# Performance work log

Hardware: AMD Instinct MI355X
Metric: run time of the kernel (lower is better)

Reference implementation:

```python
import jax, jax.numpy as jnp
import numpy as np

N_NODES = 100000
N_EDGES = 1600000
IN_DIM = 128
HID = 64
N_CLASSES = 40
NEG_SLOPE = 0.2


def setup_inputs() -> dict:
    key = jax.random.key(0)
    ks = jax.random.split(key, 12)
    s_in = 1.0 / np.sqrt(IN_DIM)
    s_h = 1.0 / np.sqrt(HID)
    return {
        "x": jax.random.normal(ks[0], (N_NODES, IN_DIM), dtype=jnp.float32),
        "edge_index": jax.random.randint(ks[1], (2, N_EDGES), 0, N_NODES, dtype=jnp.int64),
        "W0": jax.random.normal(ks[2], (IN_DIM, HID), dtype=jnp.float32) * s_in,
        "a_s0": jax.random.normal(ks[3], (HID,), dtype=jnp.float32) * s_h,
        "a_d0": jax.random.normal(ks[4], (HID,), dtype=jnp.float32) * s_h,
        "b0": jnp.zeros((HID,), dtype=jnp.float32),
        "W1": jax.random.normal(ks[5], (HID, HID), dtype=jnp.float32) * s_h,
        "a_s1": jax.random.normal(ks[6], (HID,), dtype=jnp.float32) * s_h,
        "a_d1": jax.random.normal(ks[7], (HID,), dtype=jnp.float32) * s_h,
        "b1": jnp.zeros((HID,), dtype=jnp.float32),
        "Wl": jax.random.normal(ks[8], (HID, N_CLASSES), dtype=jnp.float32) * s_h,
        "bl": jnp.zeros((N_CLASSES,), dtype=jnp.float32),
    }


def gat_conv(x, src, dst, W, a_s, a_d, b, n_nodes):
    # single-head GATConv (PyG default heads=1), self-loops already in src/dst
    h = x @ W                                  # [N, d]
    e = jax.nn.leaky_relu((h @ a_s)[src] + (h @ a_d)[dst], NEG_SLOPE)  # [E]
    # segment softmax over incoming edges of each dst node
    m = jax.ops.segment_max(e, dst, num_segments=n_nodes)
    p = jnp.exp(e - m[dst])
    denom = jax.ops.segment_sum(p, dst, num_segments=n_nodes)
    alpha = p / (denom[dst] + 1e-16)           # [E]
    out = jax.ops.segment_sum(alpha[:, None] * h[src], dst, num_segments=n_nodes)
    return out + b


def reference(x, edge_index, W0, a_s0, a_d0, b0, W1, a_s1, a_d1, b1, Wl, bl):
    n = x.shape[0]
    loop = jnp.arange(n, dtype=edge_index.dtype)
    src = jnp.concatenate([edge_index[0], loop])
    dst = jnp.concatenate([edge_index[1], loop])
    h = gat_conv(x, src, dst, W0, a_s0, a_d0, b0, n)
    h = jax.nn.elu(h)
    h = gat_conv(h, src, dst, W1, a_s1, a_d1, b1, n)
    h = jax.nn.elu(h)
    return h @ Wl + bl
```

## Files before the change

### kernel.cpp

```cpp
#include <hip/hip_runtime.h>
#include <math.h>

#define NEG_SLOPE 0.2f
#define CAP 256
#define BSH 9
#define BSZ 512
#define CHUNK 2048
#define PADS 16

typedef __attribute__((ext_vector_type(8))) short short8;
typedef __attribute__((ext_vector_type(4))) float f32x4;

__device__ __forceinline__ float hred_sum(float v) {
#pragma unroll
    for (int o = 16; o >= 1; o >>= 1) v += __shfl_xor(v, o, 64);
    return v;
}
__device__ __forceinline__ unsigned int f2bf(float f) {
    unsigned int u = __float_as_uint(f);
    return (u + 0x7fffu + ((u >> 16) & 1u)) >> 16;
}
__device__ __forceinline__ float bflo(unsigned int u) { return __uint_as_float(u << 16); }
__device__ __forceinline__ float bfhi(unsigned int u) { return __uint_as_float(u & 0xffff0000u); }


__global__ __launch_bounds__(256) void k_zero(int* p, int n) {
    int i = blockIdx.x * 256 + threadIdx.x;
    if (i < n) p[i] = 0;
}

__global__ __launch_bounds__(256) void k_hist(const int* __restrict__ dst, int* __restrict__ bcount, int E) {
    __shared__ int lh[256];
    lh[threadIdx.x] = 0;
    __syncthreads();
    int gid = blockIdx.x * 256 + threadIdx.x;
    int nth = gridDim.x * 256;
    int E4 = E >> 2;
    for (int i = gid; i < E4; i += nth) {
        int4 d = ((const int4*)dst)[i];
        atomicAdd(&lh[d.x >> BSH], 1);
        atomicAdd(&lh[d.y >> BSH], 1);
        atomicAdd(&lh[d.z >> BSH], 1);
        atomicAdd(&lh[d.w >> BSH], 1);
    }
    for (int i = (E4 << 2) + gid; i < E; i += nth)
        atomicAdd(&lh[dst[i] >> BSH], 1);
    __syncthreads();
    int c = lh[threadIdx.x];
    if (c) atomicAdd(&bcount[threadIdx.x * PADS], c);
}

__global__ __launch_bounds__(256) void k_bscan(const int* __restrict__ bcount,
                                               int* __restrict__ eoff, int* __restrict__ boff,
                                               int* __restrict__ bcursor, int* __restrict__ rowptr,
                                               int nbuck, int N, int E) {
    __shared__ int s1[256], s2[256];
    int t = threadIdx.x;
    int bc = (t < nbuck) ? bcount[t * PADS] : 0;
    int cn = 0;
    if (t < nbuck) { cn = N - (t << BSH); if (cn > BSZ) cn = BSZ; if (cn < 0) cn = 0; }
    int tot = bc + cn;
    s1[t] = bc; s2[t] = tot;
    __syncthreads();
#pragma unroll
    for (int off = 1; off < 256; off <<= 1) {
        int u1 = (t >= off) ? s1[t - off] : 0;
        int u2 = (t >= off) ? s2[t - off] : 0;
        __syncthreads();
        s1[t] += u1; s2[t] += u2;
        __syncthreads();
    }
    if (t < nbuck) {
        int e = s1[t] - bc, b = s2[t] - tot;
        eoff[t] = e; boff[t] = b; bcursor[t * PADS] = e;
    }
    if (t == 0) rowptr[N] = E + N;
}

__global__ __launch_bounds__(256) void k_scatter(const int* __restrict__ src, const int* __restrict__ dst,
                                                 int* __restrict__ bcursor, int* __restrict__ ebuf, int E) {
    __shared__ int lh[256], lb[256];
    const int tid = threadIdx.x;
    int base = blockIdx.x * CHUNK;
    int sv[8], dv[8];
    bool ok[8];
#pragma unroll
    for (int u = 0; u < 8; ++u) {
        int i = base + u * 256 + tid;
        ok[u] = i < E;
        int ii = ok[u] ? i : E - 1;
        dv[u] = dst[ii];
        sv[u] = src[ii];
    }
    lh[tid] = 0;
    __syncthreads();
#pragma unroll
    for (int u = 0; u < 8; ++u)
        if (ok[u]) atomicAdd(&lh[dv[u] >> BSH], 1);
    __syncthreads();
    int c = lh[tid];
    lb[tid] = c ? atomicAdd(&bcursor[tid * PADS], c) : 0;
    lh[tid] = 0;
    __syncthreads();
#pragma unroll
    for (int u = 0; u < 8; ++u) {
        if (ok[u]) {
            int d = dv[u], b = d >> BSH;
            int p = atomicAdd(&lh[b], 1);
            ebuf[lb[b] + p] = (sv[u] << BSH) | (d & (BSZ - 1));
        }
    }
}

__global__ __launch_bounds__(512) void k_build(const int* __restrict__ eoff, const int* __restrict__ boff,
                                               const int* __restrict__ bcount, const int* __restrict__ ebuf,
                                               int* __restrict__ rowptr, int* __restrict__ csr, int N) {
    __shared__ int sdeg[BSZ], sscan[BSZ];
    int b = blockIdx.x, t = threadIdx.x;
    int nlo = b << BSH;
    int cn = N - nlo; if (cn > BSZ) cn = BSZ;
    int e0 = eoff[b], ec = bcount[b * PADS], cb = boff[b];
    sdeg[t] = (t < cn) ? 1 : 0;
    __syncthreads();
    {
        int i = t;
        for (; i + 1536 < ec; i += 2048) {
            int r0 = ebuf[e0 + i], r1 = ebuf[e0 + i + 512];
            int r2 = ebuf[e0 + i + 1024], r3 = ebuf[e0 + i + 1536];
            atomicAdd(&sdeg[r0 & (BSZ - 1)], 1);
            atomicAdd(&sdeg[r1 & (BSZ - 1)], 1);
            atomicAdd(&sdeg[r2 & (BSZ - 1)], 1);
            atomicAdd(&sdeg[r3 & (BSZ - 1)], 1);
        }
        for (; i < ec; i += 512)
            atomicAdd(&sdeg[ebuf[e0 + i] & (BSZ - 1)], 1);
    }
    __syncthreads();
    int v = sdeg[t];
    sscan[t] = v;
    __syncthreads();
#pragma unroll
    for (int off = 1; off < BSZ; off <<= 1) {
        int u = (t >= off) ? sscan[t - off] : 0;
        __syncthreads();
        sscan[t] += u;
        __syncthreads();
    }
    int excl = sscan[t] - v;
    if (t < cn) {
        rowptr[nlo + t] = cb + excl;
        csr[cb + excl] = nlo + t;
        sdeg[t] = excl + 1;
    }
    __syncthreads();
    {
        int i = t;
        for (; i + 1536 < ec; i += 2048) {
            int r0 = ebuf[e0 + i], r1 = ebuf[e0 + i + 512];
            int r2 = ebuf[e0 + i + 1024], r3 = ebuf[e0 + i + 1536];
            int p0 = atomicAdd(&sdeg[r0 & (BSZ - 1)], 1);
            int p1 = atomicAdd(&sdeg[r1 & (BSZ - 1)], 1);
            int p2 = atomicAdd(&sdeg[r2 & (BSZ - 1)], 1);
            int p3 = atomicAdd(&sdeg[r3 & (BSZ - 1)], 1);
            csr[cb + p0] = r0 >> BSH;
            csr[cb + p1] = r1 >> BSH;
            csr[cb + p2] = r2 >> BSH;
            csr[cb + p3] = r3 >> BSH;
        }
        for (; i < ec; i += 512) {
            int rec = ebuf[e0 + i];
            int p = atomicAdd(&sdeg[rec & (BSZ - 1)], 1);
            csr[cb + p] = rec >> BSH;
        }
    }
}


template <int K, int OUTW, bool SS, bool HB>
__global__ __launch_bounds__(256) void k_gemm(const float* __restrict__ X,
                                              const float* __restrict__ W,
                                              const float* __restrict__ a_s,
                                              const float* __restrict__ a_d,
                                              const float* __restrict__ bias,
                                              void* __restrict__ Hout,
                                              float* __restrict__ ss,
                                              float* __restrict__ sd, int N) {
    constexpr int NKC = K / 32;
    constexpr int NC  = (OUTW + 15) / 16;
    __shared__ __align__(16) short wfrag[NKC * NC * 64 * 8];
    __shared__ __align__(16) unsigned int hs[HB ? 4 : 1][16 * 32];

    const int tid  = threadIdx.x;
    const int lane = tid & 63;
    const int w    = tid >> 6;
    const int m    = lane & 15;
    const int q8   = lane >> 4;
    const int rowbase = blockIdx.x * 64 + w * 16;

    for (int f = tid; f < NKC * NC * 64; f += 256) {
        int flane = f & 63;
        int fc    = (f >> 6) % NC;
        int fkc   = (f >> 6) / NC;
        int col   = fc * 16 + (flane & 15);
        int k0    = fkc * 32 + (flane >> 4) * 8;
        short8 b;
#pragma unroll
        for (int j = 0; j < 8; ++j) {
            float v = (col < OUTW) ? W[(k0 + j) * OUTW + col] : 0.f;
            b[j] = (short)f2bf(v);
        }
        *(short8*)&wfrag[f * 8] = b;
    }
    __syncthreads();

    int grow = rowbase + m; if (grow >= N) grow = N - 1;
    const float* xrow = X + (size_t)grow * K + q8 * 8;

    f32x4 acc[NC];
#pragma unroll
    for (int c = 0; c < NC; ++c) acc[c] = (f32x4)0.f;

#pragma unroll
    for (int kc = 0; kc < NKC; ++kc) {
        float4 v0 = *(const float4*)(xrow + kc * 32);
        float4 v1 = *(const float4*)(xrow + kc * 32 + 4);
        float vv[8] = {v0.x, v0.y, v0.z, v0.w, v1.x, v1.y, v1.z, v1.w};
        short8 ah, al;
#pragma unroll
        for (int j = 0; j < 8; ++j) {
            unsigned int hb16 = f2bf(vv[j]);
            ah[j] = (short)hb16;
            al[j] = (short)f2bf(vv[j] - __uint_as_float(hb16 << 16));
        }
#pragma unroll
        for (int c = 0; c < NC; ++c) {
            short8 b = *(short8*)&wfrag[((kc * NC + c) * 64 + lane) * 8];
            acc[c] = __builtin_amdgcn_mfma_f32_16x16x32_bf16(ah, b, acc[c], 0, 0, 0);
            acc[c] = __builtin_amdgcn_mfma_f32_16x16x32_bf16(al, b, acc[c], 0, 0, 0);
        }
    }

    if (SS) {
        float asv[NC], adv[NC];
#pragma unroll
        for (int c = 0; c < NC; ++c) { asv[c] = a_s[c * 16 + m]; adv[c] = a_d[c * 16 + m]; }
#pragma unroll
        for (int i = 0; i < 4; ++i) {
            float s = 0.f, d = 0.f;
#pragma unroll
            for (int c = 0; c < NC; ++c) {
                s = fmaf(acc[c][i], asv[c], s);
                d = fmaf(acc[c][i], adv[c], d);
            }
#pragma unroll
            for (int o = 1; o <= 8; o <<= 1) {
                s += __shfl_xor(s, o, 64);
                d += __shfl_xor(d, o, 64);
            }
            int r = rowbase + q8 * 4 + i;
            if (m == 0 && r < N) { ss[r] = s; sd[r] = d; }
        }
    }

    if (HB) {
        unsigned short* hsw = (unsigned short*)&hs[w][0];
#pragma unroll
        for (int c = 0; c < NC; ++c)
#pragma unroll
            for (int i = 0; i < 4; ++i)
                hsw[(q8 * 4 + i) * 64 + c * 16 + m] = (unsigned short)f2bf(acc[c][i]);
        unsigned int* hu = &hs[w][0];
        int row = lane >> 2, u0 = (lane & 3) * 8;
        uint4 va = *(uint4*)&hu[row * 32 + u0];
        uint4 vb = *(uint4*)&hu[row * 32 + u0 + 4];
        int r = rowbase + row;
        if (r < N) {
            unsigned int* hbp = (unsigned int*)Hout;
            *(uint4*)&hbp[(size_t)r * 32 + u0]     = va;
            *(uint4*)&hbp[(size_t)r * 32 + u0 + 4] = vb;
        }
    } else {
        float bv[NC];
#pragma unroll
        for (int c = 0; c < NC; ++c) {
            int col = c * 16 + m;
            bv[c] = (col < OUTW) ? bias[col] : 0.f;
        }
        float* O = (float*)Hout;
#pragma unroll
        for (int i = 0; i < 4; ++i) {
            int r = rowbase + q8 * 4 + i;
            if (r < N) {
#pragma unroll
                for (int c = 0; c < NC; ++c) {
                    int col = c * 16 + m;
                    if (col < OUTW) O[(size_t)r * OUTW + col] = acc[c][i] + bv[c];
                }
            }
        }
    }
}


__global__ __launch_bounds__(256) void k_agg(const int* __restrict__ rowptr, const int* __restrict__ csr,
                                             const float* __restrict__ ss, const float* __restrict__ sd,
                                             const unsigned int* __restrict__ hb, const float* __restrict__ bias,
                                             float* __restrict__ z, int N) {
    __shared__ float2 ps[8 * CAP];
    const int tid = threadIdx.x;
    const int hw  = tid >> 5;
    const int p   = tid & 31;
    const int n   = blockIdx.x * 8 + hw;
    const bool valid = n < N;
    float2* myps = ps + hw * CAP;
    const char* hbb = (const char*)hb;
    const int p4 = p * 4;

    int ro = 0, deg = 0;
    float sdn = 0.f;
    if (valid) {
        ro  = rowptr[n];
        deg = rowptr[n + 1] - ro;
        sdn = sd[n];
    }

    if (deg <= CAP) {
        float sum = 0.f;
        for (int j = p; j < deg; j += 32) {
            int s = csr[ro + j];
            float e = ss[s] + sdn;
            e = fmaxf(e, NEG_SLOPE * e);
            float pe = __expf(e);
            myps[j] = make_float2(pe, __int_as_float(s << 7));
            sum += pe;
        }
        sum = hred_sum(sum);
        float inv = 1.f / (sum + 1e-16f);

        float ax = 0.f, ay = 0.f, bx = 0.f, by = 0.f, cx = 0.f, cy = 0.f, dx = 0.f, dy = 0.f;
        int j = 0;
        for (; j + 7 < deg; j += 8) {
            float2 e0 = myps[j],     e1 = myps[j + 1], e2 = myps[j + 2], e3 = myps[j + 3];
            float2 e4 = myps[j + 4], e5 = myps[j + 5], e6 = myps[j + 6], e7 = myps[j + 7];
            unsigned int u0 = *(const unsigned int*)(hbb + (__float_as_int(e0.y) + p4));
            unsigned int u1 = *(const unsigned int*)(hbb + (__float_as_int(e1.y) + p4));
            unsigned int u2 = *(const unsigned int*)(hbb + (__float_as_int(e2.y) + p4));
            unsigned int u3 = *(const unsigned int*)(hbb + (__float_as_int(e3.y) + p4));
            unsigned int u4 = *(const unsigned int*)(hbb + (__float_as_int(e4.y) + p4));
            unsigned int u5 = *(const unsigned int*)(hbb + (__float_as_int(e5.y) + p4));
            unsigned int u6 = *(const unsigned int*)(hbb + (__float_as_int(e6.y) + p4));
            unsigned int u7 = *(const unsigned int*)(hbb + (__float_as_int(e7.y) + p4));
            ax = fmaf(bflo(u0), e0.x, ax); ay = fmaf(bfhi(u0), e0.x, ay);
            bx = fmaf(bflo(u1), e1.x, bx); by = fmaf(bfhi(u1), e1.x, by);
            cx = fmaf(bflo(u2), e2.x, cx); cy = fmaf(bfhi(u2), e2.x, cy);
            dx = fmaf(bflo(u3), e3.x, dx); dy = fmaf(bfhi(u3), e3.x, dy);
            ax = fmaf(bflo(u4), e4.x, ax); ay = fmaf(bfhi(u4), e4.x, ay);
            bx = fmaf(bflo(u5), e5.x, bx); by = fmaf(bfhi(u5), e5.x, by);
            cx = fmaf(bflo(u6), e6.x, cx); cy = fmaf(bfhi(u6), e6.x, cy);
            dx = fmaf(bflo(u7), e7.x, dx); dy = fmaf(bfhi(u7), e7.x, dy);
        }
        for (; j + 3 < deg; j += 4) {
            float2 e0 = myps[j], e1 = myps[j + 1], e2 = myps[j + 2], e3 = myps[j + 3];
            unsigned int u0 = *(const unsigned int*)(hbb + (__float_as_int(e0.y) + p4));
            unsigned int u1 = *(const unsigned int*)(hbb + (__float_as_int(e1.y) + p4));
            unsigned int u2 = *(const unsigned int*)(hbb + (__float_as_int(e2.y) + p4));
            unsigned int u3 = *(const unsigned int*)(hbb + (__float_as_int(e3.y) + p4));
            ax = fmaf(bflo(u0), e0.x, ax); ay = fmaf(bfhi(u0), e0.x, ay);
            bx = fmaf(bflo(u1), e1.x, bx); by = fmaf(bfhi(u1), e1.x, by);
            cx = fmaf(bflo(u2), e2.x, cx); cy = fmaf(bfhi(u2), e2.x, cy);
            dx = fmaf(bflo(u3), e3.x, dx); dy = fmaf(bfhi(u3), e3.x, dy);
        }
        for (; j < deg; ++j) {
            float2 e0 = myps[j];
            unsigned int u0 = *(const unsigned int*)(hbb + (__float_as_int(e0.y) + p4));
            ax = fmaf(bflo(u0), e0.x, ax); ay = fmaf(bfhi(u0), e0.x, ay);
        }
        float fx = (ax + bx) + (cx + dx);
        float fy = (ay + by) + (cy + dy);
        if (valid) {
            float2 ob = *(const float2*)&bias[p * 2];
            float ox = fmaf(fx, inv, ob.x);
            float oy = fmaf(fy, inv, ob.y);
            ox = (ox > 0.f) ? ox : __expf(ox) - 1.f;
            oy = (oy > 0.f) ? oy : __expf(oy) - 1.f;
            *(float2*)&z[(size_t)n * 64 + p * 2] = make_float2(ox, oy);
        }
    } else {
        float sum = 0.f;
        for (int j = p; j < deg; j += 32) {
            int s = csr[ro + j];
            float e = ss[s] + sdn;
            e = fmaxf(e, NEG_SLOPE * e);
            sum += __expf(e);
        }
        sum = hred_sum(sum);
        float inv = 1.f / (sum + 1e-16f);
        float fx = 0.f, fy = 0.f;
        for (int j = 0; j < deg; ++j) {
            int s = csr[ro + j];
            float e = ss[s] + sdn;
            e = fmaxf(e, NEG_SLOPE * e);
            float pe = __expf(e);
            unsigned int u = *(const unsigned int*)(hbb + ((s << 7) + p4));
            fx = fmaf(bflo(u), pe, fx); fy = fmaf(bfhi(u), pe, fy);
        }
        float2 ob = *(const float2*)&bias[p * 2];
        float ox = fmaf(fx, inv, ob.x);
        float oy = fmaf(fy, inv, ob.y);
        ox = (ox > 0.f) ? ox : __expf(ox) - 1.f;
        oy = (oy > 0.f) ? oy : __expf(oy) - 1.f;
        *(float2*)&z[(size_t)n * 64 + p * 2] = make_float2(ox, oy);
    }
}


extern "C" void kernel_launch(void* const* d_in, const int* in_sizes, int n_in,
                              void* d_out, int out_size, void* d_ws, size_t ws_size,
                              hipStream_t stream) {
    const float* x   = (const float*)d_in[0];
    const int*   ei  = (const int*)d_in[1];
    const float* W0  = (const float*)d_in[2];
    const float* as0 = (const float*)d_in[3];
    const float* ad0 = (const float*)d_in[4];
    const float* b0  = (const float*)d_in[5];
    const float* W1  = (const float*)d_in[6];
    const float* as1 = (const float*)d_in[7];
    const float* ad1 = (const float*)d_in[8];
    const float* b1  = (const float*)d_in[9];
    const float* Wl  = (const float*)d_in[10];
    const float* bl  = (const float*)d_in[11];
    float* out = (float*)d_out;

    int N = in_sizes[0] / 128;
    int E = in_sizes[1] / 2;
    const int* srcp = ei;
    const int* dstp = ei + E;
    int nbuck = (N + BSZ - 1) >> BSH;

    char* wp = (char*)d_ws;
    auto alloc = [&](size_t bytes) { void* p = (void*)wp; wp += (bytes + 255) & ~(size_t)255; return p; };
    unsigned int* hb = (unsigned int*)alloc((size_t)N * 32 * 4);
    float* z       = (float*)alloc((size_t)N * 64 * 4);
    float* ssb     = (float*)alloc((size_t)N * 4);
    float* sdb     = (float*)alloc((size_t)N * 4);
    int*   rowptr  = (int*)alloc((size_t)(N + 1) * 4);
    int*   csr     = (int*)alloc((size_t)(E + N) * 4);
    int*   ebuf    = (int*)alloc((size_t)E * 4);
    int*   bcount  = (int*)alloc(256 * PADS * 4);
    int*   eoff    = (int*)alloc(256 * 4);
    int*   boff    = (int*)alloc(256 * 4);
    int*   bcursor = (int*)alloc(256 * PADS * 4);

    k_zero<<<(256 * PADS + 255) / 256, 256, 0, stream>>>(bcount, 256 * PADS);
    k_hist<<<256, 256, 0, stream>>>(dstp, bcount, E);
    k_bscan<<<1, 256, 0, stream>>>(bcount, eoff, boff, bcursor, rowptr, nbuck, N, E);
    k_scatter<<<(E + CHUNK - 1) / CHUNK, 256, 0, stream>>>(srcp, dstp, bcursor, ebuf, E);
    k_build<<<nbuck, 512, 0, stream>>>(eoff, boff, bcount, ebuf, rowptr, csr, N);

    int gb = (N + 63) / 64;
    k_gemm<128, 64, true, true><<<gb, 256, 0, stream>>>(x, W0, as0, ad0, nullptr, hb, ssb, sdb, N);
    k_agg<<<(N + 7) / 8, 256, 0, stream>>>(rowptr, csr, ssb, sdb, hb, b0, z, N);
    k_gemm<64, 64, true, true><<<gb, 256, 0, stream>>>(z, W1, as1, ad1, nullptr, hb, ssb, sdb, N);
    k_agg<<<(N + 7) / 8, 256, 0, stream>>>(rowptr, csr, ssb, sdb, hb, b1, z, N);
    k_gemm<64, 40, false, false><<<gb, 256, 0, stream>>>(z, Wl, nullptr, nullptr, bl, out, nullptr, nullptr, N);
}
```

Before: 271.5 us.

## Store aggregation outputs as bf16 and drop atomic histogram reduction

The aggregation kernel now writes its ELU outputs as packed bf16 instead of fp32. The following GEMMs read that bf16 directly and issue one MFMA per tile instead of a hi/lo split pair. This halves intermediate traffic and MFMA work but lowers activation precision. The histogram now writes per-block partials that the scan kernel sums, removing the zero kernel and global atomics. The aggregation's shared-memory staging is split into separate weight and offset arrays so it can use vector loads.

```diff
diff --git a/kernel.cpp b/kernel.cpp
--- a/kernel.cpp
+++ b/kernel.cpp
@@ -7,6 +7,7 @@
 #define BSZ 512
 #define CHUNK 2048
 #define PADS 16
+#define HGRID 256
 
 typedef __attribute__((ext_vector_type(8))) short short8;
 typedef __attribute__((ext_vector_type(4))) float f32x4;
@@ -24,12 +25,7 @@
 __device__ __forceinline__ float bfhi(unsigned int u) { return __uint_as_float(u & 0xffff0000u); }
 
 
-__global__ __launch_bounds__(256) void k_zero(int* p, int n) {
-    int i = blockIdx.x * 256 + threadIdx.x;
-    if (i < n) p[i] = 0;
-}
-
-__global__ __launch_bounds__(256) void k_hist(const int* __restrict__ dst, int* __restrict__ bcount, int E) {
+__global__ __launch_bounds__(256) void k_hist(const int* __restrict__ dst, int* __restrict__ bpart, int E) {
     __shared__ int lh[256];
     lh[threadIdx.x] = 0;
     __syncthreads();
@@ -46,17 +42,24 @@
     for (int i = (E4 << 2) + gid; i < E; i += nth)
         atomicAdd(&lh[dst[i] >> BSH], 1);
     __syncthreads();
-    int c = lh[threadIdx.x];
-    if (c) atomicAdd(&bcount[threadIdx.x * PADS], c);
-}
-
-__global__ __launch_bounds__(256) void k_bscan(const int* __restrict__ bcount,
+    bpart[blockIdx.x * 256 + threadIdx.x] = lh[threadIdx.x];
+}
+
+__global__ __launch_bounds__(256) void k_bscan(const int* __restrict__ bpart,
                                                int* __restrict__ eoff, int* __restrict__ boff,
-                                               int* __restrict__ bcursor, int* __restrict__ rowptr,
+                                               int* __restrict__ bcursor, int* __restrict__ ecnt,
+                                               int* __restrict__ rowptr,
                                                int nbuck, int N, int E) {
     __shared__ int s1[256], s2[256];
     int t = threadIdx.x;
-    int bc = (t < nbuck) ? bcount[t * PADS] : 0;
+    int bc = 0;
+    for (int b = 0; b < HGRID; b += 4) {
+        bc += bpart[(b + 0) * 256 + t];
+        bc += bpart[(b + 1) * 256 + t];
+        bc += bpart[(b + 2) * 256 + t];
+        bc += bpart[(b + 3) * 256 + t];
+    }
+    if (t >= nbuck) bc = 0;
     int cn = 0;
     if (t < nbuck) { cn = N - (t << BSH); if (cn > BSZ) cn = BSZ; if (cn < 0) cn = 0; }
     int tot = bc + cn;
@@ -72,7 +75,7 @@
     }
     if (t < nbuck) {
         int e = s1[t] - bc, b = s2[t] - tot;
-        eoff[t] = e; boff[t] = b; bcursor[t * PADS] = e;
+        eoff[t] = e; boff[t] = b; ecnt[t] = bc; bcursor[t * PADS] = e;
     }
     if (t == 0) rowptr[N] = E + N;
 }
@@ -113,13 +116,13 @@
 }
 
 __global__ __launch_bounds__(512) void k_build(const int* __restrict__ eoff, const int* __restrict__ boff,
-                                               const int* __restrict__ bcount, const int* __restrict__ ebuf,
+                                               const int* __restrict__ ecnt, const int* __restrict__ ebuf,
                                                int* __restrict__ rowptr, int* __restrict__ csr, int N) {
     __shared__ int sdeg[BSZ], sscan[BSZ];
     int b = blockIdx.x, t = threadIdx.x;
     int nlo = b << BSH;
     int cn = N - nlo; if (cn > BSZ) cn = BSZ;
-    int e0 = eoff[b], ec = bcount[b * PADS], cb = boff[b];
+    int e0 = eoff[b], ec = ecnt[b], cb = boff[b];
     sdeg[t] = (t < cn) ? 1 : 0;
     __syncthreads();
     {
@@ -176,8 +179,8 @@
 }
 
 
-template <int K, int OUTW, bool SS, bool HB>
-__global__ __launch_bounds__(256) void k_gemm(const float* __restrict__ X,
+template <int K, int OUTW, bool SS, bool HB, bool XB>
+__global__ __launch_bounds__(256) void k_gemm(const void* __restrict__ X,
                                               const float* __restrict__ W,
                                               const float* __restrict__ a_s,
                                               const float* __restrict__ a_d,
@@ -214,29 +217,42 @@
     __syncthreads();
 
     int grow = rowbase + m; if (grow >= N) grow = N - 1;
-    const float* xrow = X + (size_t)grow * K + q8 * 8;
 
     f32x4 acc[NC];
 #pragma unroll
     for (int c = 0; c < NC; ++c) acc[c] = (f32x4)0.f;
 
-#pragma unroll
-    for (int kc = 0; kc < NKC; ++kc) {
-        float4 v0 = *(const float4*)(xrow + kc * 32);
-        float4 v1 = *(const float4*)(xrow + kc * 32 + 4);
-        float vv[8] = {v0.x, v0.y, v0.z, v0.w, v1.x, v1.y, v1.z, v1.w};
-        short8 ah, al;
-#pragma unroll
-        for (int j = 0; j < 8; ++j) {
-            unsigned int hb16 = f2bf(vv[j]);
-            ah[j] = (short)hb16;
-            al[j] = (short)f2bf(vv[j] - __uint_as_float(hb16 << 16));
-        }
-#pragma unroll
-        for (int c = 0; c < NC; ++c) {
-            short8 b = *(short8*)&wfrag[((kc * NC + c) * 64 + lane) * 8];
-            acc[c] = __builtin_amdgcn_mfma_f32_16x16x32_bf16(ah, b, acc[c], 0, 0, 0);
-            acc[c] = __builtin_amdgcn_mfma_f32_16x16x32_bf16(al, b, acc[c], 0, 0, 0);
+    if (XB) {
+        const unsigned short* xrow = (const unsigned short*)X + (size_t)grow * 64 + q8 * 8;
+#pragma unroll
+        for (int kc = 0; kc < NKC; ++kc) {
+            short8 ah = *(const short8*)(xrow + kc * 32);
+#pragma unroll
+            for (int c = 0; c < NC; ++c) {
+                short8 b = *(short8*)&wfrag[((kc * NC + c) * 64 + lane) * 8];
+                acc[c] = __builtin_amdgcn_mfma_f32_16x16x32_bf16(ah, b, acc[c], 0, 0, 0);
+            }
+        }
+    } else {
+        const float* xrow = (const float*)X + (size_t)grow * K + q8 * 8;
+#pragma unroll
+        for (int kc = 0; kc < NKC; ++kc) {
+            float4 v0 = *(const float4*)(xrow + kc * 32);
+            float4 v1 = *(const float4*)(xrow + kc * 32 + 4);
+            float vv[8] = {v0.x, v0.y, v0.z, v0.w, v1.x, v1.y, v1.z, v1.w};
+            short8 ah, al;
+#pragma unroll
+            for (int j = 0; j < 8; ++j) {
+                unsigned int hb16 = f2bf(vv[j]);
+                ah[j] = (short)hb16;
+                al[j] = (short)f2bf(vv[j] - __uint_as_float(hb16 << 16));
+            }
+#pragma unroll
+            for (int c = 0; c < NC; ++c) {
+                short8 b = *(short8*)&wfrag[((kc * NC + c) * 64 + lane) * 8];
+                acc[c] = __builtin_amdgcn_mfma_f32_16x16x32_bf16(ah, b, acc[c], 0, 0, 0);
+                acc[c] = __builtin_amdgcn_mfma_f32_16x16x32_bf16(al, b, acc[c], 0, 0, 0);
+            }
         }
     }
 
@@ -305,14 +321,14 @@
 __global__ __launch_bounds__(256) void k_agg(const int* __restrict__ rowptr, const int* __restrict__ csr,
                                              const float* __restrict__ ss, const float* __restrict__ sd,
                                              const unsigned int* __restrict__ hb, const float* __restrict__ bias,
-                                             float* __restrict__ z, int N) {
-    __shared__ float2 ps[8 * CAP];
+                                             unsigned int* __restrict__ z, int N) {
+    __shared__ __align__(16) float sal[8][CAP];
+    __shared__ __align__(16) int   sof[8][CAP];
     const int tid = threadIdx.x;
     const int hw  = tid >> 5;
     const int p   = tid & 31;
     const int n   = blockIdx.x * 8 + hw;
     const bool valid = n < N;
-    float2* myps = ps + hw * CAP;
     const char* hbb = (const char*)hb;
     const int p4 = p * 4;
 
@@ -331,7 +347,8 @@
             float e = ss[s] + sdn;
             e = fmaxf(e, NEG_SLOPE * e);
             float pe = __expf(e);
-            myps[j] = make_float2(pe, __int_as_float(s << 7));
+            sal[hw][j] = pe;
+            sof[hw][j] = s << 7;
             sum += pe;
         }
         sum = hred_sum(sum);
@@ -340,40 +357,43 @@
         float ax = 0.f, ay = 0.f, bx = 0.f, by = 0.f, cx = 0.f, cy = 0.f, dx = 0.f, dy = 0.f;
         int j = 0;
         for (; j + 7 < deg; j += 8) {
-            float2 e0 = myps[j],     e1 = myps[j + 1], e2 = myps[j + 2], e3 = myps[j + 3];
-            float2 e4 = myps[j + 4], e5 = myps[j + 5], e6 = myps[j + 6], e7 = myps[j + 7];
-            unsigned int u0 = *(const unsigned int*)(hbb + (__float_as_int(e0.y) + p4));
-            unsigned int u1 = *(const unsigned int*)(hbb + (__float_as_int(e1.y) + p4));
-            unsigned int u2 = *(const unsigned int*)(hbb + (__float_as_int(e2.y) + p4));
-            unsigned int u3 = *(const unsigned int*)(hbb + (__float_as_int(e3.y) + p4));
-            unsigned int u4 = *(const unsigned int*)(hbb + (__float_as_int(e4.y) + p4));
-            unsigned int u5 = *(const unsigned int*)(hbb + (__float_as_int(e5.y) + p4));
-            unsigned int u6 = *(const unsigned int*)(hbb + (__float_as_int(e6.y) + p4));
-            unsigned int u7 = *(const unsigned int*)(hbb + (__float_as_int(e7.y) + p4));
-            ax = fmaf(bflo(u0), e0.x, ax); ay = fmaf(bfhi(u0), e0.x, ay);
-            bx = fmaf(bflo(u1), e1.x, bx); by = fmaf(bfhi(u1), e1.x, by);
-            cx = fmaf(bflo(u2), e2.x, cx); cy = fmaf(bfhi(u2), e2.x, cy);
-            dx = fmaf(bflo(u3), e3.x, dx); dy = fmaf(bfhi(u3), e3.x, dy);
-            ax = fmaf(bflo(u4), e4.x, ax); ay = fmaf(bfhi(u4), e4.x, ay);
-            bx = fmaf(bflo(u5), e5.x, bx); by = fmaf(bfhi(u5), e5.x, by);
-            cx = fmaf(bflo(u6), e6.x, cx); cy = fmaf(bfhi(u6), e6.x, cy);
-            dx = fmaf(bflo(u7), e7.x, dx); dy = fmaf(bfhi(u7), e7.x, dy);
+            float4 al0 = *(const float4*)&sal[hw][j];
+            float4 al1 = *(const float4*)&sal[hw][j + 4];
+            int4   of0 = *(const int4*)&sof[hw][j];
+            int4   of1 = *(const int4*)&sof[hw][j + 4];
+            unsigned int u0 = *(const unsigned int*)(hbb + (of0.x + p4));
+            unsigned int u1 = *(const unsigned int*)(hbb + (of0.y + p4));
+            unsigned int u2 = *(const unsigned int*)(hbb + (of0.z + p4));
+            unsigned int u3 = *(const unsigned int*)(hbb + (of0.w + p4));
+            unsigned int u4 = *(const unsigned int*)(hbb + (of1.x + p4));
+            unsigned int u5 = *(const unsigned int*)(hbb + (of1.y + p4));
+            unsigned int u6 = *(const unsigned int*)(hbb + (of1.z + p4));
+            unsigned int u7 = *(const unsigned int*)(hbb + (of1.w + p4));
+            ax = fmaf(bflo(u0), al0.x, ax); ay = fmaf(bfhi(u0), al0.x, ay);
+            bx = fmaf(bflo(u1), al0.y, bx); by = fmaf(bfhi(u1), al0.y, by);
+            cx = fmaf(bflo(u2), al0.z, cx); cy = fmaf(bfhi(u2), al0.z, cy);
+            dx = fmaf(bflo(u3), al0.w, dx); dy = fmaf(bfhi(u3), al0.w, dy);
+            ax = fmaf(bflo(u4), al1.x, ax); ay = fmaf(bfhi(u4), al1.x, ay);
+            bx = fmaf(bflo(u5), al1.y, bx); by = fmaf(bfhi(u5), al1.y, by);
+            cx = fmaf(bflo(u6), al1.z, cx); cy = fmaf(bfhi(u6), al1.z, cy);
+            dx = fmaf(bflo(u7), al1.w, dx); dy = fmaf(bfhi(u7), al1.w, dy);
         }
         for (; j + 3 < deg; j += 4) {
-            float2 e0 = myps[j], e1 = myps[j + 1], e2 = myps[j + 2], e3 = myps[j + 3];
-            unsigned int u0 = *(const unsigned int*)(hbb + (__float_as_int(e0.y) + p4));
-            unsigned int u1 = *(const unsigned int*)(hbb + (__float_as_int(e1.y) + p4));
-            unsigned int u2 = *(const unsigned int*)(hbb + (__float_as_int(e2.y) + p4));
-            unsigned int u3 = *(const unsigned int*)(hbb + (__float_as_int(e3.y) + p4));
-            ax = fmaf(bflo(u0), e0.x, ax); ay = fmaf(bfhi(u0), e0.x, ay);
-            bx = fmaf(bflo(u1), e1.x, bx); by = fmaf(bfhi(u1), e1.x, by);
-            cx = fmaf(bflo(u2), e2.x, cx); cy = fmaf(bfhi(u2), e2.x, cy);
-            dx = fmaf(bflo(u3), e3.x, dx); dy = fmaf(bfhi(u3), e3.x, dy);
+            float4 al0 = *(const float4*)&sal[hw][j];
+            int4   of0 = *(const int4*)&sof[hw][j];
+            unsigned int u0 = *(const unsigned int*)(hbb + (of0.x + p4));
+            unsigned int u1 = *(const unsigned int*)(hbb + (of0.y + p4));
+            unsigned int u2 = *(const unsigned int*)(hbb + (of0.z + p4));
+            unsigned int u3 = *(const unsigned int*)(hbb + (of0.w + p4));
+            ax = fmaf(bflo(u0), al0.x, ax); ay = fmaf(bfhi(u0), al0.x, ay);
+            bx = fmaf(bflo(u1), al0.y, bx); by = fmaf(bfhi(u1), al0.y, by);
+            cx = fmaf(bflo(u2), al0.z, cx); cy = fmaf(bfhi(u2), al0.z, cy);
+            dx = fmaf(bflo(u3), al0.w, dx); dy = fmaf(bfhi(u3), al0.w, dy);
         }
         for (; j < deg; ++j) {
-            float2 e0 = myps[j];
-            unsigned int u0 = *(const unsigned int*)(hbb + (__float_as_int(e0.y) + p4));
-            ax = fmaf(bflo(u0), e0.x, ax); ay = fmaf(bfhi(u0), e0.x, ay);
+            float a = sal[hw][j];
+            unsigned int u0 = *(const unsigned int*)(hbb + (sof[hw][j] + p4));
+            ax = fmaf(bflo(u0), a, ax); ay = fmaf(bfhi(u0), a, ay);
         }
         float fx = (ax + bx) + (cx + dx);
         float fy = (ay + by) + (cy + dy);
@@ -383,7 +403,7 @@
             float oy = fmaf(fy, inv, ob.y);
             ox = (ox > 0.f) ? ox : __expf(ox) - 1.f;
             oy = (oy > 0.f) ? oy : __expf(oy) - 1.f;
-            *(float2*)&z[(size_t)n * 64 + p * 2] = make_float2(ox, oy);
+            z[(size_t)n * 32 + p] = (f2bf(oy) << 16) | f2bf(ox);
         }
     } else {
         float sum = 0.f;
@@ -409,7 +429,7 @@
         float oy = fmaf(fy, inv, ob.y);
         ox = (ox > 0.f) ? ox : __expf(ox) - 1.f;
         oy = (oy > 0.f) ? oy : __expf(oy) - 1.f;
-        *(float2*)&z[(size_t)n * 64 + p * 2] = make_float2(ox, oy);
+        z[(size_t)n * 32 + p] = (f2bf(oy) << 16) | f2bf(ox);
     }
 }
 
@@ -440,27 +460,27 @@
     char* wp = (char*)d_ws;
     auto alloc = [&](size_t bytes) { void* p = (void*)wp; wp += (bytes + 255) & ~(size_t)255; return p; };
     unsigned int* hb = (unsigned int*)alloc((size_t)N * 32 * 4);
-    float* z       = (float*)alloc((size_t)N * 64 * 4);
+    unsigned int* z  = (unsigned int*)alloc((size_t)N * 32 * 4);
     float* ssb     = (float*)alloc((size_t)N * 4);
     float* sdb     = (float*)alloc((size_t)N * 4);
     int*   rowptr  = (int*)alloc((size_t)(N + 1) * 4);
     int*   csr     = (int*)alloc((size_t)(E + N) * 4);
     int*   ebuf    = (int*)alloc((size_t)E * 4);
-    int*   bcount  = (int*)alloc(256 * PADS * 4);
+    int*   bpart   = (int*)alloc((size_t)HGRID * 256 * 4);
     int*   eoff    = (int*)alloc(256 * 4);
     int*   boff    = (int*)alloc(256 * 4);
+    int*   ecnt    = (int*)alloc(256 * 4);
     int*   bcursor = (int*)alloc(256 * PADS * 4);
 
-    k_zero<<<(256 * PADS + 255) / 256, 256, 0, stream>>>(bcount, 256 * PADS);
-    k_hist<<<256, 256, 0, stream>>>(dstp, bcount, E);
-    k_bscan<<<1, 256, 0, stream>>>(bcount, eoff, boff, bcursor, rowptr, nbuck, N, E);
+    k_hist<<<HGRID, 256, 0, stream>>>(dstp, bpart, E);
+    k_bscan<<<1, 256, 0, stream>>>(bpart, eoff, boff, bcursor, ecnt, rowptr, nbuck, N, E);
     k_scatter<<<(E + CHUNK - 1) / CHUNK, 256, 0, stream>>>(srcp, dstp, bcursor, ebuf, E);
-    k_build<<<nbuck, 512, 0, stream>>>(eoff, boff, bcount, ebuf, rowptr, csr, N);
+    k_build<<<nbuck, 512, 0, stream>>>(eoff, boff, ecnt, ebuf, rowptr, csr, N);
 
     int gb = (N + 63) / 64;
-    k_gemm<128, 64, true, true><<<gb, 256, 0, stream>>>(x, W0, as0, ad0, nullptr, hb, ssb, sdb, N);
+    k_gemm<128, 64, true, true, false><<<gb, 256, 0, stream>>>(x, W0, as0, ad0, nullptr, hb, ssb, sdb, N);
     k_agg<<<(N + 7) / 8, 256, 0, stream>>>(rowptr, csr, ssb, sdb, hb, b0, z, N);
-    k_gemm<64, 64, true, true><<<gb, 256, 0, stream>>>(z, W1, as1, ad1, nullptr, hb, ssb, sdb, N);
+    k_gemm<64, 64, true, true, true><<<gb, 256, 0, stream>>>(z, W1, as1, ad1, nullptr, hb, ssb, sdb, N);
     k_agg<<<(N + 7) / 8, 256, 0, stream>>>(rowptr, csr, ssb, sdb, hb, b1, z, N);
-    k_gemm<64, 40, false, false><<<gb, 256, 0, stream>>>(z, Wl, nullptr, nullptr, bl, out, nullptr, nullptr, N);
-}
+    k_gemm<64, 40, false, false, true><<<gb, 256, 0, stream>>>(z, Wl, nullptr, nullptr, bl, out, nullptr, nullptr, N);
+}
```

New measurement: 266.6 us. Within noise of the previous version (-1.8%).
